# Kernel tuning notes

Hardware: AMD Instinct MI355X
Metric: run time of the kernel (lower is better)

Reference implementation:

```python
import jax, jax.numpy as jnp
import numpy as np

G = 4          # num_groups == num_kv_groups


def _proj(W, b, xf):
    # 1x1 Conv3d == per-voxel linear: xf is [b, c, N]
    return jnp.einsum('oc,bcn->bon', W, xf) + b[None, :, None]


def setup_inputs() -> dict:
    key = jax.random.key(0)
    ks = jax.random.split(key, 5)
    c = 512
    x = jax.random.normal(ks[0], (2, c, 16, 16, 16), dtype=jnp.float32)
    s = 1.0 / np.sqrt(c)
    Wq = jax.random.normal(ks[1], (c, c), dtype=jnp.float32) * s
    Wk = jax.random.normal(ks[2], (c, c), dtype=jnp.float32) * s
    Wv = jax.random.normal(ks[3], (c, c), dtype=jnp.float32) * s
    Wo = jax.random.normal(ks[4], (c, c), dtype=jnp.float32) * s
    z = jnp.zeros((c,), dtype=jnp.float32)
    return {"x": x, "Wq": Wq, "bq": z, "Wk": Wk, "bk": z, "Wv": Wv, "bv": z, "Wo": Wo, "bo": z}


def reference(x, Wq, bq, Wk, bk, Wv, bv, Wo, bo):
    b, c, d, h, w = x.shape
    N = d * h * w
    gs = c // G                       # head (group) dim
    scale = gs ** -0.5
    xf = x.reshape(b, c, N)           # [b, c, N]
    q = _proj(Wq, bq, xf).reshape(b, G, gs, N).transpose(0, 1, 3, 2)  # [b,G,N,gs]
    k = _proj(Wk, bk, xf).reshape(b, G, gs, N).transpose(0, 1, 3, 2)
    v = _proj(Wv, bv, xf).reshape(b, G, gs, N).transpose(0, 1, 3, 2)
    sim = jnp.einsum('bgqd,bgkd->bgqk', q, k) * scale  # [b,G,N,N]
    attn = jax.nn.softmax(sim, axis=-1)
    out = jnp.einsum('bgqk,bgkd->bgqd', attn, v)       # [b,G,N,gs]
    out = out.transpose(0, 1, 3, 2).reshape(b, c, N)   # [b,c,N]
    out = _proj(Wo, bo, out).reshape(b, c, d, h, w)
    return x + out
```

## Files before the change

### kernel.cpp

```cpp
#include <hip/hip_runtime.h>
#include <hip/hip_bf16.h>
#include <stdint.h>

#define B_ 2
#define C_ 512
#define G_ 4
#define D_ 128
#define N_ 4096

typedef __bf16 bf16;
typedef __bf16 bf16x8 __attribute__((ext_vector_type(8)));
typedef float  f32x4  __attribute__((ext_vector_type(4)));
typedef float  f32x16 __attribute__((ext_vector_type(16)));

#define MFMA   __builtin_amdgcn_mfma_f32_16x16x32_bf16
#define MFMA32 __builtin_amdgcn_mfma_f32_32x32x16_bf16

#define SWZ(row, c) ((((c) ^ (((row) >> 1) & 3)) << 4))

#define OFF_Q   (0u)
#define OFF_K   (8388608u)
#define OFF_VT  (16777216u)
#define OFF_XT  (25165824u)
#define OFF_WB  (33554432u)
#define OFF_OP  (35651584u)
#define OFF_ML  (52428800u)
#define WS_NEED_SPLIT (52953088u)

__device__ inline unsigned pk2(float a, float b) {
    union { bf16 h[2]; unsigned u; } t;
    t.h[0] = (bf16)a; t.h[1] = (bf16)b;
    return t.u;
}
__device__ inline void pl32(unsigned &a, unsigned &b) {
    asm volatile("v_permlane32_swap_b32 %0, %1" : "+v"(a), "+v"(b));
}
__device__ inline void gload16(const char* src, char* lds) {
    __builtin_amdgcn_global_load_lds(
        (const __attribute__((address_space(1))) unsigned*)src,
        (__attribute__((address_space(3))) unsigned*)lds, 16, 0, 0);
}
__device__ inline float max3f(float a, float b, float c) {
    return fmaxf(fmaxf(a, b), c);
}

__global__ __launch_bounds__(256) void wcvt_kernel(const float* __restrict__ Wq,
                                                   const float* __restrict__ Wk,
                                                   const float* __restrict__ Wv,
                                                   const float* __restrict__ Wo,
                                                   bf16* __restrict__ out) {
    int m = blockIdx.y;
    const float* W = (m == 0) ? Wq : (m == 1) ? Wk : (m == 2) ? Wv : Wo;
    int i = (blockIdx.x * 256 + threadIdx.x) * 4;
    float4 v = *(const float4*)(W + i);
    union { bf16 h[4]; uint2 u; } pk;
    pk.h[0] = (bf16)v.x; pk.h[1] = (bf16)v.y; pk.h[2] = (bf16)v.z; pk.h[3] = (bf16)v.w;
    *(uint2*)(out + (size_t)m * (C_ * C_) + i) = pk.u;
}

__global__ __launch_bounds__(256) void xt_kernel(const float* __restrict__ x,
                                                 bf16* __restrict__ xT) {
    __shared__ bf16 t[64 * 80];
    int n0 = blockIdx.x * 64, c0 = blockIdx.y * 64, b = blockIdx.z;
    const float* xp = x + (size_t)b * C_ * N_;
#pragma unroll
    for (int i = 0; i < 16; ++i) {
        int idx = threadIdx.x + 256 * i;
        int cl = idx >> 6, nl = idx & 63;
        float v = xp[(size_t)(c0 + cl) * N_ + n0 + nl];
        t[nl * 80 + cl] = (bf16)v;
    }
    __syncthreads();
    bf16* xt = xT + ((size_t)b * N_ + n0) * C_ + c0;
#pragma unroll
    for (int i = 0; i < 2; ++i) {
        int id = threadIdx.x + 256 * i;
        int nl = id >> 3, c8 = (id & 7) * 8;
        *(uint4*)(xt + (size_t)nl * C_ + c8) = *(const uint4*)(t + nl * 80 + c8);
    }
}

__global__ __launch_bounds__(256) void qkv_kernel(const bf16* __restrict__ xT,
                                                  const bf16* __restrict__ WB,
                                                  const float* __restrict__ bq,
                                                  const float* __restrict__ bk,
                                                  const float* __restrict__ bv,
                                                  bf16* __restrict__ Q,
                                                  bf16* __restrict__ K,
                                                  bf16* __restrict__ Vt) {
    __shared__ char smem[32768];
    const int tid = threadIdx.x;
    const int w = tid >> 6, l = tid & 63;
    const int lr = l & 15, lg = l >> 4;
    const int wr = w >> 1, wc = w & 1;
    const int mat = blockIdx.z;
    const bf16* A = xT;
    const bf16* W = WB + (size_t)mat * (C_ * C_);
    const float* bias = (mat == 0) ? bq : (mat == 1) ? bk : bv;
    const int r0 = blockIdx.x * 128, o0 = blockIdx.y * 128;
    const float QSCALE = 0.08838834764831845f * 1.4426950408889634f;

    const char* srcA[2]; const char* srcB[2]; int dA[2], dB[2];
#pragma unroll
    for (int i = 0; i < 2; ++i) {
        int CL = tid + 256 * i, row = CL >> 2, c = CL & 3;
        srcA[i] = (const char*)(A + (size_t)(r0 + row) * C_) + SWZ(row, c);
        srcB[i] = (const char*)(W + (size_t)(o0 + row) * C_) + SWZ(row, c);
        dA[i] = CL << 4;
        dB[i] = 8192 + (CL << 4);
    }

    f32x4 z = {0.f, 0.f, 0.f, 0.f};
    f32x4 acc[4][4];
#pragma unroll
    for (int m = 0; m < 4; ++m)
#pragma unroll
        for (int n = 0; n < 4; ++n) acc[m][n] = z;

    auto STAGE = [&](int buf, int kt) {
        char* base = smem + buf * 16384;
        int kb = kt * 64;
#pragma unroll
        for (int i = 0; i < 2; ++i) {
            gload16(srcA[i] + kb, base + dA[i]);
            gload16(srcB[i] + kb, base + dB[i]);
        }
    };

    STAGE(0, 0);
    __syncthreads();
#pragma unroll 4
    for (int t = 0; t < 16; ++t) {
        int cur = t & 1;
        if (t < 15) STAGE(cur ^ 1, t + 1);
        char* Ab = smem + cur * 16384;
        char* Bb = Ab + 8192;
        bf16x8 af[4], bg_[4];
#pragma unroll
        for (int m = 0; m < 4; ++m) {
            int row = wr * 64 + m * 16 + lr;
            af[m] = *(const bf16x8*)(Ab + row * 64 + SWZ(row, lg));
        }
#pragma unroll
        for (int n = 0; n < 4; ++n) {
            int row = wc * 64 + n * 16 + lr;
            bg_[n] = *(const bf16x8*)(Bb + row * 64 + SWZ(row, lg));
        }
#pragma unroll
        for (int m = 0; m < 4; ++m)
#pragma unroll
            for (int n = 0; n < 4; ++n)
                acc[m][n] = MFMA(af[m], bg_[n], acc[m][n], 0, 0, 0);
        __syncthreads();
    }

#pragma unroll
    for (int n = 0; n < 4; ++n) {
        int o = o0 + wc * 64 + n * 16 + lr;
        float bs = bias[o];
        int g = o >> 7, d = o & 127;
#pragma unroll
        for (int m = 0; m < 4; ++m) {
            int row = r0 + wr * 64 + m * 16 + lg * 4;
            int b = row >> 12, nn = row & (N_ - 1);
            if (mat == 0) {
#pragma unroll
                for (int j = 0; j < 4; ++j)
                    Q[((size_t)(b * G_ + g) * N_ + nn + j) * D_ + d] =
                        (bf16)((acc[m][n][j] + bs) * QSCALE);
            } else if (mat == 1) {
#pragma unroll
                for (int j = 0; j < 4; ++j)
                    K[((size_t)(b * G_ + g) * N_ + nn + j) * D_ + d] =
                        (bf16)(acc[m][n][j] + bs);
            } else {
                union { bf16 h[4]; uint2 u; } pk;
#pragma unroll
                for (int j = 0; j < 4; ++j) pk.h[j] = (bf16)(acc[m][n][j] + bs);
                *(uint2*)(Vt + ((size_t)(b * G_ + g) * D_ + d) * N_ + nn) = pk.u;
            }
        }
    }
}

template<int SPLITS>
__global__ __launch_bounds__(512, 2) void attn_kernel(const bf16* __restrict__ Q,
                                                      const bf16* __restrict__ K,
                                                      const bf16* __restrict__ Vt,
                                                      bf16* __restrict__ XT,
                                                      bf16* __restrict__ Op,
                                                      float* __restrict__ ML) {
    __shared__ char smem[65536];
    const int tid = threadIdx.x;
    const int w = tid >> 6, l = tid & 63;
    const int l31 = l & 31, h = l >> 5;

    const int L = blockIdx.x;
    const int bg = L & 7;
    const int ix = L >> 3;
    const int sp = (SPLITS > 1) ? (ix >> 4) : 0;
    const int qb = (SPLITS > 1) ? (ix & 15) : ix;

    const bf16* Qh = Q + (size_t)bg * N_ * D_;
    const char* Kh = (const char*)(K + (size_t)bg * N_ * D_);
    const char* Vh = (const char*)(Vt + (size_t)bg * D_ * N_);
    const int q0 = qb * 256 + w * 32;
    const int kv0 = sp * (N_ / SPLITS);
    const int NT = N_ / SPLITS / 64;

    int offK[2], offV[2];
#pragma unroll
    for (int j = 0; j < 2; ++j) {
        int CL = (w * 2 + j) * 64 + l;
        int row = CL >> 4;
        int cp = (CL & 15) ^ (row & 15);
        offK[j] = row * 256 + cp * 16;
        int dv = 2 * row + (cp >> 3), k8 = cp & 7;
        offV[j] = dv * (N_ * 2) + k8 * 16;
    }

    bf16x8 aq[8];
#pragma unroll
    for (int kb = 0; kb < 8; ++kb)
        aq[kb] = *(const bf16x8*)(Qh + (size_t)(q0 + l31) * D_ + kb * 16 + h * 8);

    bf16 one_ = (bf16)1.0f;
    bf16x8 ones = {one_, one_, one_, one_, one_, one_, one_, one_};

    f32x16 oacc[4], lacc;
#pragma unroll
    for (int dt = 0; dt < 4; ++dt)
#pragma unroll
        for (int r = 0; r < 16; ++r) oacc[dt][r] = 0.f;
#pragma unroll
    for (int r = 0; r < 16; ++r) lacc[r] = 0.f;
    float mrun = -1e30f;
    const float THR = 5.0f;

    auto STAGE = [&](int buf, int kv) {
        const char* pk = Kh + (size_t)kv * 256;
        const char* pv = Vh + (size_t)kv * 2;
        char* kb = smem + buf * 32768 + w * 2048;
        char* vb = smem + buf * 32768 + 16384 + w * 2048;
#pragma unroll
        for (int j = 0; j < 2; ++j) gload16(pk + offK[j], kb + j * 1024);
#pragma unroll
        for (int j = 0; j < 2; ++j) gload16(pv + offV[j], vb + j * 1024);
    };

    STAGE(0, kv0);

    for (int t = 0; t < NT; ++t) {
        int cur = t & 1;
        __builtin_amdgcn_s_barrier();
        if (t + 1 < NT) {
            STAGE(cur ^ 1, kv0 + (t + 1) * 64);
            asm volatile("s_waitcnt vmcnt(4)" ::: "memory");
        } else {
            asm volatile("s_waitcnt vmcnt(0)" ::: "memory");
        }
        __builtin_amdgcn_sched_barrier(0);
        __builtin_amdgcn_s_barrier();
        char* Kb = smem + cur * 32768;
        char* Vb = smem + cur * 32768 + 16384;

        f32x16 s0, s1;
#pragma unroll
        for (int r = 0; r < 16; ++r) { s0[r] = 0.f; s1[r] = 0.f; }
        __builtin_amdgcn_s_setprio(1);
#pragma unroll
        for (int kb = 0; kb < 8; ++kb) {
            int ch = (((kb << 1) | h) ^ (l31 & 15)) << 4;
            bf16x8 kf0 = *(const bf16x8*)(Kb + (size_t)l31 * 256 + ch);
            s0 = MFMA32(kf0, aq[kb], s0, 0, 0, 0);
            bf16x8 kf1 = *(const bf16x8*)(Kb + (size_t)(32 + l31) * 256 + ch);
            s1 = MFMA32(kf1, aq[kb], s1, 0, 0, 0);
        }
        __builtin_amdgcn_s_setprio(0);

        float x0 = max3f(s0[0],  s0[1],  s0[2]);
        float x1 = max3f(s0[3],  s0[4],  s0[5]);
        float x2 = max3f(s0[6],  s0[7],  s0[8]);
        float x3 = max3f(s0[9],  s0[10], s0[11]);
        float x4 = max3f(s0[12], s0[13], s0[14]);
        float x5 = max3f(s0[15], s1[0],  s1[1]);
        float x6 = max3f(s1[2],  s1[3],  s1[4]);
        float x7 = max3f(s1[5],  s1[6],  s1[7]);
        float x8 = max3f(s1[8],  s1[9],  s1[10]);
        float x9 = max3f(s1[11], s1[12], s1[13]);
        float xa = fmaxf(s1[14], s1[15]);
        float y0 = max3f(x0, x1, x2);
        float y1 = max3f(x3, x4, x5);
        float y2 = max3f(x6, x7, x8);
        float y3 = fmaxf(x9, xa);
        float mt = fmaxf(max3f(y0, y1, y2), y3);
        mt = fmaxf(mt, __shfl_xor(mt, 32));

        if (__any(mt > mrun + THR)) {
            float mn = fmaxf(mrun, mt);
            float corr = __builtin_amdgcn_exp2f(mrun - mn);
            mrun = mn;
#pragma unroll
            for (int r = 0; r < 16; ++r) {
                int qr = (r & 3) + 8 * (r >> 2) + 4 * h;
                float cr = __shfl(corr, qr);
                lacc[r] *= cr;
#pragma unroll
                for (int dt = 0; dt < 4; ++dt) oacc[dt][r] *= cr;
            }
        }

#pragma unroll
        for (int r = 0; r < 16; ++r) {
            s0[r] = __builtin_amdgcn_exp2f(s0[r] - mrun);
            s1[r] = __builtin_amdgcn_exp2f(s1[r] - mrun);
        }

        bf16x8 pa0, pa1, pa2, pa3;
        {
            unsigned x0_ = pk2(s0[0], s0[1]),  y0_ = pk2(s0[4], s0[5]);  pl32(x0_, y0_);
            unsigned x1_ = pk2(s0[2], s0[3]),  y1_ = pk2(s0[6], s0[7]);  pl32(x1_, y1_);
            pa0 = __builtin_bit_cast(bf16x8, (uint4){x0_, x1_, y0_, y1_});
            unsigned x2_ = pk2(s0[8], s0[9]),  y2_ = pk2(s0[12], s0[13]); pl32(x2_, y2_);
            unsigned x3_ = pk2(s0[10], s0[11]), y3_ = pk2(s0[14], s0[15]); pl32(x3_, y3_);
            pa1 = __builtin_bit_cast(bf16x8, (uint4){x2_, x3_, y2_, y3_});
            unsigned x4_ = pk2(s1[0], s1[1]),  y4_ = pk2(s1[4], s1[5]);  pl32(x4_, y4_);
            unsigned x5_ = pk2(s1[2], s1[3]),  y5_ = pk2(s1[6], s1[7]);  pl32(x5_, y5_);
            pa2 = __builtin_bit_cast(bf16x8, (uint4){x4_, x5_, y4_, y5_});
            unsigned x6_ = pk2(s1[8], s1[9]),  y6_ = pk2(s1[12], s1[13]); pl32(x6_, y6_);
            unsigned x7_ = pk2(s1[10], s1[11]), y7_ = pk2(s1[14], s1[15]); pl32(x7_, y7_);
            pa3 = __builtin_bit_cast(bf16x8, (uint4){x6_, x7_, y6_, y7_});
        }

        __builtin_amdgcn_s_setprio(1);
#pragma unroll
        for (int sl = 0; sl < 4; ++sl) {
            bf16x8 pa = (sl == 0) ? pa0 : (sl == 1) ? pa1 : (sl == 2) ? pa2 : pa3;
#pragma unroll
            for (int dt = 0; dt < 4; ++dt) {
                int row = dt * 16 + (l31 >> 1);
                int ch = ((((l31 & 1) << 3) + (sl << 1) + h) ^ (l31 >> 1)) << 4;
                bf16x8 vf = *(const bf16x8*)(Vb + (size_t)row * 256 + ch);
                oacc[dt] = MFMA32(pa, vf, oacc[dt], 0, 0, 0);
            }
            lacc = MFMA32(pa, ones, lacc, 0, 0, 0);
        }
        __builtin_amdgcn_s_setprio(0);
    }

    if (SPLITS > 1) {
        float2* mlp = (float2*)ML + ((size_t)sp * 8 + bg) * N_ + q0;
#pragma unroll
        for (int r = 0; r < 16; ++r) {
            int qr = (r & 3) + 8 * (r >> 2) + 4 * h;
            float mv = __shfl(mrun, qr);
            if (l31 == 0) {
                float2 v; v.x = mv; v.y = lacc[r];
                mlp[qr] = v;
            }
        }
        bf16* op = Op + (((size_t)sp * 8 + bg) * N_ + q0) * D_;
#pragma unroll
        for (int dt = 0; dt < 4; ++dt)
#pragma unroll
            for (int r = 0; r < 16; ++r) {
                int qr = (r & 3) + 8 * (r >> 2) + 4 * h;
                op[(size_t)qr * D_ + dt * 32 + l31] = (bf16)oacc[dt][r];
            }
    } else {
        int b = bg >> 2, g = bg & 3;
#pragma unroll
        for (int r = 0; r < 16; ++r) {
            int qr = (r & 3) + 8 * (r >> 2) + 4 * h;
            float iv = 1.f / lacc[r];
#pragma unroll
            for (int dt = 0; dt < 4; ++dt)
                XT[((size_t)b * N_ + q0 + qr) * C_ + g * D_ + dt * 32 + l31] =
                    (bf16)(oacc[dt][r] * iv);
        }
    }
}

template<int FUSE>
__global__ __launch_bounds__(256) void oproj_kernel(const bf16* __restrict__ Ob,
                                                    const bf16* __restrict__ Op,
                                                    const float* __restrict__ ML,
                                                    const bf16* __restrict__ WB,
                                                    const float* __restrict__ bo,
                                                    const float* __restrict__ x,
                                                    float* __restrict__ out) {
    __shared__ char smem[24576];
    const int tid = threadIdx.x;
    const int w = tid >> 6, l = tid & 63;
    const int lr = l & 15, lg = l >> 4;
    const int wr = w >> 1, wc = w & 1;
    const bf16* W = WB + (size_t)3 * (C_ * C_);
    const int r0 = blockIdx.x * 128, o0 = blockIdx.y * 64;

    const char* srcA[2]; int dA[2], cpw[2]; size_t opRow[2];
    float w0f[2][4], w1f[2][4];
#pragma unroll
    for (int i = 0; i < 2; ++i) {
        int CL = tid + 256 * i, row = CL >> 2, c = CL & 3;
        cpw[i] = c ^ ((row >> 1) & 3);
        dA[i] = CL << 4;
        srcA[i] = (const char*)(Ob + (size_t)(r0 + row) * C_) + (cpw[i] << 4);
        if (FUSE) {
            int rg = r0 + row;
            int b = rg >> 12, n = rg & (N_ - 1);
            const float2* mlp = (const float2*)ML;
#pragma unroll
            for (int g = 0; g < 4; ++g) {
                int bg = b * 4 + g;
                float2 ml0 = mlp[(size_t)bg * N_ + n];
                float2 ml1 = mlp[(size_t)(8 + bg) * N_ + n];
                float mm = fmaxf(ml0.x, ml1.x);
                float a0 = __builtin_amdgcn_exp2f(ml0.x - mm);
                float a1 = __builtin_amdgcn_exp2f(ml1.x - mm);
                float inv = 1.f / (a0 * ml0.y + a1 * ml1.y);
                w0f[i][g] = a0 * inv;
                w1f[i][g] = a1 * inv;
            }
            opRow[i] = ((size_t)(b * 4) * N_ + n) * 256u;
        }
    }
    const char* srcB; int dB;
    {
        int CL = tid, row = CL >> 2, c = CL & 3;
        srcB = (const char*)(W + (size_t)(o0 + row) * C_) + SWZ(row, c);
        dB = 8192 + (CL << 4);
    }

    f32x4 z = {0.f, 0.f, 0.f, 0.f};
    f32x4 acc[4][2];
#pragma unroll
    for (int m = 0; m < 4; ++m) { acc[m][0] = z; acc[m][1] = z; }

    uint4 a0r[2], a1r[2];
    auto LOAD_A = [&](int kt) {
        int g = kt >> 2;
#pragma unroll
        for (int i = 0; i < 2; ++i) {
            size_t off = opRow[i] + (size_t)g * ((size_t)N_ * 256u - 256u)
                       + (size_t)(kt * 64) + ((size_t)cpw[i] << 4);
            a0r[i] = *(const uint4*)((const char*)Op + off);
            a1r[i] = *(const uint4*)((const char*)Op + 8388608u + off);
        }
    };
    auto WRITE_A = [&](int buf, int kt) {
        int g = kt >> 2;
        char* base = smem + buf * 12288;
#pragma unroll
        for (int i = 0; i < 2; ++i) {
            union { uint4 u; bf16 h[8]; } u0, u1, uo;
            u0.u = a0r[i]; u1.u = a1r[i];
#pragma unroll
            for (int e = 0; e < 8; ++e)
                uo.h[e] = (bf16)(w0f[i][g] * (float)u0.h[e] + w1f[i][g] * (float)u1.h[e]);
            *(uint4*)(base + dA[i]) = uo.u;
        }
    };
    auto STAGE_A_PLAIN = [&](int buf, int kt) {
        char* base = smem + buf * 12288;
#pragma unroll
        for (int i = 0; i < 2; ++i) gload16(srcA[i] + kt * 64, base + dA[i]);
    };
    auto STAGE_B = [&](int buf, int kt) {
        gload16(srcB + kt * 64, smem + buf * 12288 + dB);
    };

    STAGE_B(0, 0);
    if (FUSE) { LOAD_A(0); WRITE_A(0, 0); }
    else       STAGE_A_PLAIN(0, 0);
    __syncthreads();

    for (int t = 0; t < 16; ++t) {
        int cur = t & 1;
        if (t < 15) {
            STAGE_B(cur ^ 1, t + 1);
            if (FUSE) LOAD_A(t + 1);
            else      STAGE_A_PLAIN(cur ^ 1, t + 1);
        }
        char* Ab = smem + cur * 12288;
        char* Bb = Ab + 8192;
        bf16x8 af[4], bg_[2];
#pragma unroll
        for (int m = 0; m < 4; ++m) {
            int row = wr * 64 + m * 16 + lr;
            af[m] = *(const bf16x8*)(Ab + row * 64 + SWZ(row, lg));
        }
#pragma unroll
        for (int n = 0; n < 2; ++n) {
            int row = wc * 32 + n * 16 + lr;
            bg_[n] = *(const bf16x8*)(Bb + row * 64 + SWZ(row, lg));
        }
#pragma unroll
        for (int m = 0; m < 4; ++m)
#pragma unroll
            for (int n = 0; n < 2; ++n)
                acc[m][n] = MFMA(af[m], bg_[n], acc[m][n], 0, 0, 0);
        if (FUSE && t < 15) WRITE_A(cur ^ 1, t + 1);
        __syncthreads();
    }

#pragma unroll
    for (int n = 0; n < 2; ++n) {
        int o = o0 + wc * 32 + n * 16 + lr;
        float bs = bo[o];
#pragma unroll
        for (int m = 0; m < 4; ++m) {
            int row = r0 + wr * 64 + m * 16 + lg * 4;
            int b = row >> 12, nn = row & (N_ - 1);
            size_t base = ((size_t)b * C_ + o) * N_ + nn;
            float4 xv = *(const float4*)(x + base);
            float4 ov;
            ov.x = acc[m][n][0] + bs + xv.x;
            ov.y = acc[m][n][1] + bs + xv.y;
            ov.z = acc[m][n][2] + bs + xv.z;
            ov.w = acc[m][n][3] + bs + xv.w;
            *(float4*)(out + base) = ov;
        }
    }
}

extern "C" void kernel_launch(void* const* d_in, const int* in_sizes, int n_in,
                              void* d_out, int out_size, void* d_ws, size_t ws_size,
                              hipStream_t stream) {
    const float* x  = (const float*)d_in[0];
    const float* Wq = (const float*)d_in[1];
    const float* bq = (const float*)d_in[2];
    const float* Wk = (const float*)d_in[3];
    const float* bk = (const float*)d_in[4];
    const float* Wv = (const float*)d_in[5];
    const float* bv = (const float*)d_in[6];
    const float* Wo = (const float*)d_in[7];
    const float* bo = (const float*)d_in[8];

    char* ws = (char*)d_ws;
    bf16* Q   = (bf16*)(ws + OFF_Q);
    bf16* K   = (bf16*)(ws + OFF_K);
    bf16* Vt  = (bf16*)(ws + OFF_VT);
    bf16* XT  = (bf16*)(ws + OFF_XT);
    bf16* WB  = (bf16*)(ws + OFF_WB);
    bf16* Op  = (bf16*)(ws + OFF_OP);
    float* ML = (float*)(ws + OFF_ML);
    float* out = (float*)d_out;

    hipLaunchKernelGGL(wcvt_kernel, dim3(256, 4), dim3(256), 0, stream, Wq, Wk, Wv, Wo, WB);
    hipLaunchKernelGGL(xt_kernel, dim3(64, 8, 2), dim3(256), 0, stream, x, XT);
    hipLaunchKernelGGL(qkv_kernel, dim3(64, 4, 3), dim3(256), 0, stream,
                       XT, WB, bq, bk, bv, Q, K, Vt);
    if (ws_size >= (size_t)WS_NEED_SPLIT) {
        hipLaunchKernelGGL(attn_kernel<2>, dim3(256), dim3(512), 0, stream,
                           Q, K, Vt, XT, Op, ML);
        hipLaunchKernelGGL(oproj_kernel<1>, dim3(64, 8), dim3(256), 0, stream,
                           XT, Op, ML, WB, bo, x, out);
    } else {
        hipLaunchKernelGGL(attn_kernel<1>, dim3(128), dim3(512), 0, stream,
                           Q, K, Vt, XT, Op, ML);
        hipLaunchKernelGGL(oproj_kernel<0>, dim3(64, 8), dim3(256), 0, stream,
                           XT, Op, ML, WB, bo, x, out);
    }
}
```

Baseline: 131.9 us.

## Stage 128-key KV tiles per barrier in new big-LDS attention kernel

Adds an attention kernel that uses 128KB of dynamic shared memory to double-buffer 128-key KV chunks, so each pair of barriers covers two 64-key sub-tiles. The goal is to halve the barrier and wait count per key and keep more loads in flight. In exchange occupancy drops to one 512-thread block per CU instead of two, which may reduce latency hiding across blocks. The tile body is factored into shared helpers, and the old kernel remains as a fallback if the shared-memory attribute cannot be set.

```diff
diff --git a/kernel.cpp b/kernel.cpp
--- a/kernel.cpp
+++ b/kernel.cpp
@@ -183,6 +183,123 @@
     }
 }
 
+struct AttnState {
+    f32x16 oacc[4], lacc;
+    float mrun;
+};
+
+template<typename T>
+__device__ inline void attn_tile_body(AttnState& st, const bf16x8* aq,
+                                      const bf16x8& ones, char* Kb, char* Vb,
+                                      int l31, int h, T) {
+    const float THR = 5.0f;
+    f32x16 s0, s1;
+#pragma unroll
+    for (int r = 0; r < 16; ++r) { s0[r] = 0.f; s1[r] = 0.f; }
+    __builtin_amdgcn_s_setprio(1);
+#pragma unroll
+    for (int kb = 0; kb < 8; ++kb) {
+        int ch = (((kb << 1) | h) ^ (l31 & 15)) << 4;
+        bf16x8 kf0 = *(const bf16x8*)(Kb + (size_t)l31 * 256 + ch);
+        s0 = MFMA32(kf0, aq[kb], s0, 0, 0, 0);
+        bf16x8 kf1 = *(const bf16x8*)(Kb + (size_t)(32 + l31) * 256 + ch);
+        s1 = MFMA32(kf1, aq[kb], s1, 0, 0, 0);
+    }
+    __builtin_amdgcn_s_setprio(0);
+
+    float x0 = max3f(s0[0],  s0[1],  s0[2]);
+    float x1 = max3f(s0[3],  s0[4],  s0[5]);
+    float x2 = max3f(s0[6],  s0[7],  s0[8]);
+    float x3 = max3f(s0[9],  s0[10], s0[11]);
+    float x4 = max3f(s0[12], s0[13], s0[14]);
+    float x5 = max3f(s0[15], s1[0],  s1[1]);
+    float x6 = max3f(s1[2],  s1[3],  s1[4]);
+    float x7 = max3f(s1[5],  s1[6],  s1[7]);
+    float x8 = max3f(s1[8],  s1[9],  s1[10]);
+    float x9 = max3f(s1[11], s1[12], s1[13]);
+    float xa = fmaxf(s1[14], s1[15]);
+    float y0 = max3f(x0, x1, x2);
+    float y1 = max3f(x3, x4, x5);
+    float y2 = max3f(x6, x7, x8);
+    float y3 = fmaxf(x9, xa);
+    float mt = fmaxf(max3f(y0, y1, y2), y3);
+    mt = fmaxf(mt, __shfl_xor(mt, 32));
+
+    if (__any(mt > st.mrun + THR)) {
+        float mn = fmaxf(st.mrun, mt);
+        float corr = __builtin_amdgcn_exp2f(st.mrun - mn);
+        st.mrun = mn;
+#pragma unroll
+        for (int r = 0; r < 16; ++r) {
+            int qr = (r & 3) + 8 * (r >> 2) + 4 * h;
+            float cr = __shfl(corr, qr);
+            st.lacc[r] *= cr;
+#pragma unroll
+            for (int dt = 0; dt < 4; ++dt) st.oacc[dt][r] *= cr;
+        }
+    }
+
+#pragma unroll
+    for (int r = 0; r < 16; ++r) {
+        s0[r] = __builtin_amdgcn_exp2f(s0[r] - st.mrun);
+        s1[r] = __builtin_amdgcn_exp2f(s1[r] - st.mrun);
+    }
+
+    bf16x8 pa0, pa1, pa2, pa3;
+    {
+        unsigned u0 = pk2(s0[0], s0[1]),  v0 = pk2(s0[4], s0[5]);  pl32(u0, v0);
+        unsigned u1 = pk2(s0[2], s0[3]),  v1 = pk2(s0[6], s0[7]);  pl32(u1, v1);
+        pa0 = __builtin_bit_cast(bf16x8, (uint4){u0, u1, v0, v1});
+        unsigned u2 = pk2(s0[8], s0[9]),  v2 = pk2(s0[12], s0[13]); pl32(u2, v2);
+        unsigned u3 = pk2(s0[10], s0[11]), v3 = pk2(s0[14], s0[15]); pl32(u3, v3);
+        pa1 = __builtin_bit_cast(bf16x8, (uint4){u2, u3, v2, v3});
+        unsigned u4 = pk2(s1[0], s1[1]),  v4 = pk2(s1[4], s1[5]);  pl32(u4, v4);
+        unsigned u5 = pk2(s1[2], s1[3]),  v5 = pk2(s1[6], s1[7]);  pl32(u5, v5);
+        pa2 = __builtin_bit_cast(bf16x8, (uint4){u4, u5, v4, v5});
+        unsigned u6 = pk2(s1[8], s1[9]),  v6 = pk2(s1[12], s1[13]); pl32(u6, v6);
+        unsigned u7 = pk2(s1[10], s1[11]), v7 = pk2(s1[14], s1[15]); pl32(u7, v7);
+        pa3 = __builtin_bit_cast(bf16x8, (uint4){u6, u7, v6, v7});
+    }
+
+    __builtin_amdgcn_s_setprio(1);
+#pragma unroll
+    for (int sl = 0; sl < 4; ++sl) {
+        bf16x8 pa = (sl == 0) ? pa0 : (sl == 1) ? pa1 : (sl == 2) ? pa2 : pa3;
+#pragma unroll
+        for (int dt = 0; dt < 4; ++dt) {
+            int row = dt * 16 + (l31 >> 1);
+            int ch = ((((l31 & 1) << 3) + (sl << 1) + h) ^ (l31 >> 1)) << 4;
+            bf16x8 vf = *(const bf16x8*)(Vb + (size_t)row * 256 + ch);
+            st.oacc[dt] = MFMA32(pa, vf, st.oacc[dt], 0, 0, 0);
+        }
+        st.lacc = MFMA32(pa, ones, st.lacc, 0, 0, 0);
+    }
+    __builtin_amdgcn_s_setprio(0);
+}
+
+__device__ inline void attn_epilogue(AttnState& st, int sp, int bg, int q0,
+                                     int l, int l31, int h,
+                                     bf16* Op, float* ML) {
+    float2* mlp = (float2*)ML + ((size_t)sp * 8 + bg) * N_ + q0;
+#pragma unroll
+    for (int r = 0; r < 16; ++r) {
+        int qr = (r & 3) + 8 * (r >> 2) + 4 * h;
+        float mv = __shfl(st.mrun, qr);
+        if (l31 == 0) {
+            float2 v; v.x = mv; v.y = st.lacc[r];
+            mlp[qr] = v;
+        }
+    }
+    bf16* op = Op + (((size_t)sp * 8 + bg) * N_ + q0) * D_;
+#pragma unroll
+    for (int dt = 0; dt < 4; ++dt)
+#pragma unroll
+        for (int r = 0; r < 16; ++r) {
+            int qr = (r & 3) + 8 * (r >> 2) + 4 * h;
+            op[(size_t)qr * D_ + dt * 32 + l31] = (bf16)st.oacc[dt][r];
+        }
+}
+
 template<int SPLITS>
 __global__ __launch_bounds__(512, 2) void attn_kernel(const bf16* __restrict__ Q,
                                                       const bf16* __restrict__ K,
@@ -227,15 +344,14 @@
     bf16 one_ = (bf16)1.0f;
     bf16x8 ones = {one_, one_, one_, one_, one_, one_, one_, one_};
 
-    f32x16 oacc[4], lacc;
+    AttnState st;
 #pragma unroll
     for (int dt = 0; dt < 4; ++dt)
 #pragma unroll
-        for (int r = 0; r < 16; ++r) oacc[dt][r] = 0.f;
-#pragma unroll
-    for (int r = 0; r < 16; ++r) lacc[r] = 0.f;
-    float mrun = -1e30f;
-    const float THR = 5.0f;
+        for (int r = 0; r < 16; ++r) st.oacc[dt][r] = 0.f;
+#pragma unroll
+    for (int r = 0; r < 16; ++r) st.lacc[r] = 0.f;
+    st.mrun = -1e30f;
 
     auto STAGE = [&](int buf, int kv) {
         const char* pk = Kh + (size_t)kv * 256;
@@ -261,124 +377,112 @@
         }
         __builtin_amdgcn_sched_barrier(0);
         __builtin_amdgcn_s_barrier();
-        char* Kb = smem + cur * 32768;
-        char* Vb = smem + cur * 32768 + 16384;
-
-        f32x16 s0, s1;
-#pragma unroll
-        for (int r = 0; r < 16; ++r) { s0[r] = 0.f; s1[r] = 0.f; }
-        __builtin_amdgcn_s_setprio(1);
-#pragma unroll
-        for (int kb = 0; kb < 8; ++kb) {
-            int ch = (((kb << 1) | h) ^ (l31 & 15)) << 4;
-            bf16x8 kf0 = *(const bf16x8*)(Kb + (size_t)l31 * 256 + ch);
-            s0 = MFMA32(kf0, aq[kb], s0, 0, 0, 0);
-            bf16x8 kf1 = *(const bf16x8*)(Kb + (size_t)(32 + l31) * 256 + ch);
-            s1 = MFMA32(kf1, aq[kb], s1, 0, 0, 0);
-        }
-        __builtin_amdgcn_s_setprio(0);
-
-        float x0 = max3f(s0[0],  s0[1],  s0[2]);
-        float x1 = max3f(s0[3],  s0[4],  s0[5]);
-        float x2 = max3f(s0[6],  s0[7],  s0[8]);
-        float x3 = max3f(s0[9],  s0[10], s0[11]);
-        float x4 = max3f(s0[12], s0[13], s0[14]);
-        float x5 = max3f(s0[15], s1[0],  s1[1]);
-        float x6 = max3f(s1[2],  s1[3],  s1[4]);
-        float x7 = max3f(s1[5],  s1[6],  s1[7]);
-        float x8 = max3f(s1[8],  s1[9],  s1[10]);
-        float x9 = max3f(s1[11], s1[12], s1[13]);
-        float xa = fmaxf(s1[14], s1[15]);
-        float y0 = max3f(x0, x1, x2);
-        float y1 = max3f(x3, x4, x5);
-        float y2 = max3f(x6, x7, x8);
-        float y3 = fmaxf(x9, xa);
-        float mt = fmaxf(max3f(y0, y1, y2), y3);
-        mt = fmaxf(mt, __shfl_xor(mt, 32));
-
-        if (__any(mt > mrun + THR)) {
-            float mn = fmaxf(mrun, mt);
-            float corr = __builtin_amdgcn_exp2f(mrun - mn);
-            mrun = mn;
-#pragma unroll
-            for (int r = 0; r < 16; ++r) {
-                int qr = (r & 3) + 8 * (r >> 2) + 4 * h;
-                float cr = __shfl(corr, qr);
-                lacc[r] *= cr;
-#pragma unroll
-                for (int dt = 0; dt < 4; ++dt) oacc[dt][r] *= cr;
-            }
-        }
-
-#pragma unroll
-        for (int r = 0; r < 16; ++r) {
-            s0[r] = __builtin_amdgcn_exp2f(s0[r] - mrun);
-            s1[r] = __builtin_amdgcn_exp2f(s1[r] - mrun);
-        }
-
-        bf16x8 pa0, pa1, pa2, pa3;
-        {
-            unsigned x0_ = pk2(s0[0], s0[1]),  y0_ = pk2(s0[4], s0[5]);  pl32(x0_, y0_);
-            unsigned x1_ = pk2(s0[2], s0[3]),  y1_ = pk2(s0[6], s0[7]);  pl32(x1_, y1_);
-            pa0 = __builtin_bit_cast(bf16x8, (uint4){x0_, x1_, y0_, y1_});
-            unsigned x2_ = pk2(s0[8], s0[9]),  y2_ = pk2(s0[12], s0[13]); pl32(x2_, y2_);
-            unsigned x3_ = pk2(s0[10], s0[11]), y3_ = pk2(s0[14], s0[15]); pl32(x3_, y3_);
-            pa1 = __builtin_bit_cast(bf16x8, (uint4){x2_, x3_, y2_, y3_});
-            unsigned x4_ = pk2(s1[0], s1[1]),  y4_ = pk2(s1[4], s1[5]);  pl32(x4_, y4_);
-            unsigned x5_ = pk2(s1[2], s1[3]),  y5_ = pk2(s1[6], s1[7]);  pl32(x5_, y5_);
-            pa2 = __builtin_bit_cast(bf16x8, (uint4){x4_, x5_, y4_, y5_});
-            unsigned x6_ = pk2(s1[8], s1[9]),  y6_ = pk2(s1[12], s1[13]); pl32(x6_, y6_);
-            unsigned x7_ = pk2(s1[10], s1[11]), y7_ = pk2(s1[14], s1[15]); pl32(x7_, y7_);
-            pa3 = __builtin_bit_cast(bf16x8, (uint4){x6_, x7_, y6_, y7_});
-        }
-
-        __builtin_amdgcn_s_setprio(1);
-#pragma unroll
-        for (int sl = 0; sl < 4; ++sl) {
-            bf16x8 pa = (sl == 0) ? pa0 : (sl == 1) ? pa1 : (sl == 2) ? pa2 : pa3;
-#pragma unroll
-            for (int dt = 0; dt < 4; ++dt) {
-                int row = dt * 16 + (l31 >> 1);
-                int ch = ((((l31 & 1) << 3) + (sl << 1) + h) ^ (l31 >> 1)) << 4;
-                bf16x8 vf = *(const bf16x8*)(Vb + (size_t)row * 256 + ch);
-                oacc[dt] = MFMA32(pa, vf, oacc[dt], 0, 0, 0);
-            }
-            lacc = MFMA32(pa, ones, lacc, 0, 0, 0);
-        }
-        __builtin_amdgcn_s_setprio(0);
+        attn_tile_body(st, aq, ones, smem + cur * 32768,
+                       smem + cur * 32768 + 16384, l31, h, 0);
     }
 
     if (SPLITS > 1) {
-        float2* mlp = (float2*)ML + ((size_t)sp * 8 + bg) * N_ + q0;
+        attn_epilogue(st, sp, bg, q0, l, l31, h, Op, ML);
+    } else {
+        int b = bg >> 2, g = bg & 3;
 #pragma unroll
         for (int r = 0; r < 16; ++r) {
             int qr = (r & 3) + 8 * (r >> 2) + 4 * h;
-            float mv = __shfl(mrun, qr);
-            if (l31 == 0) {
-                float2 v; v.x = mv; v.y = lacc[r];
-                mlp[qr] = v;
-            }
-        }
-        bf16* op = Op + (((size_t)sp * 8 + bg) * N_ + q0) * D_;
-#pragma unroll
-        for (int dt = 0; dt < 4; ++dt)
-#pragma unroll
-            for (int r = 0; r < 16; ++r) {
-                int qr = (r & 3) + 8 * (r >> 2) + 4 * h;
-                op[(size_t)qr * D_ + dt * 32 + l31] = (bf16)oacc[dt][r];
-            }
-    } else {
-        int b = bg >> 2, g = bg & 3;
-#pragma unroll
-        for (int r = 0; r < 16; ++r) {
-            int qr = (r & 3) + 8 * (r >> 2) + 4 * h;
-            float iv = 1.f / lacc[r];
+            float iv = 1.f / st.lacc[r];
 #pragma unroll
             for (int dt = 0; dt < 4; ++dt)
                 XT[((size_t)b * N_ + q0 + qr) * C_ + g * D_ + dt * 32 + l31] =
-                    (bf16)(oacc[dt][r] * iv);
-        }
-    }
+                    (bf16)(st.oacc[dt][r] * iv);
+        }
+    }
+}
+
+__global__ __launch_bounds__(512, 1) void attn_big_kernel(const bf16* __restrict__ Q,
+                                                          const bf16* __restrict__ K,
+                                                          const bf16* __restrict__ Vt,
+                                                          bf16* __restrict__ Op,
+                                                          float* __restrict__ ML) {
+    extern __shared__ char smem[];
+    const int tid = threadIdx.x;
+    const int w = tid >> 6, l = tid & 63;
+    const int l31 = l & 31, h = l >> 5;
+
+    const int L = blockIdx.x;
+    const int bg = L & 7;
+    const int ix = L >> 3;
+    const int sp = ix >> 4;
+    const int qb = ix & 15;
+
+    const bf16* Qh = Q + (size_t)bg * N_ * D_;
+    const char* Kh = (const char*)(K + (size_t)bg * N_ * D_);
+    const char* Vh = (const char*)(Vt + (size_t)bg * D_ * N_);
+    const int q0 = qb * 256 + w * 32;
+    const int kv0 = sp * (N_ / 2);
+    const int NT = (N_ / 2) / 128;
+
+    int offK[2], offV[2];
+#pragma unroll
+    for (int j = 0; j < 2; ++j) {
+        int CL = (w * 2 + j) * 64 + l;
+        int row = CL >> 4;
+        int cp = (CL & 15) ^ (row & 15);
+        offK[j] = row * 256 + cp * 16;
+        int dv = 2 * row + (cp >> 3), k8 = cp & 7;
+        offV[j] = dv * (N_ * 2) + k8 * 16;
+    }
+
+    bf16x8 aq[8];
+#pragma unroll
+    for (int kb = 0; kb < 8; ++kb)
+        aq[kb] = *(const bf16x8*)(Qh + (size_t)(q0 + l31) * D_ + kb * 16 + h * 8);
+
+    bf16 one_ = (bf16)1.0f;
+    bf16x8 ones = {one_, one_, one_, one_, one_, one_, one_, one_};
+
+    AttnState st;
+#pragma unroll
+    for (int dt = 0; dt < 4; ++dt)
+#pragma unroll
+        for (int r = 0; r < 16; ++r) st.oacc[dt][r] = 0.f;
+#pragma unroll
+    for (int r = 0; r < 16; ++r) st.lacc[r] = 0.f;
+    st.mrun = -1e30f;
+
+    auto STAGE = [&](int buf, int kv) {
+#pragma unroll
+        for (int s2 = 0; s2 < 2; ++s2) {
+            const char* pk = Kh + (size_t)(kv + 64 * s2) * 256;
+            const char* pv = Vh + (size_t)(kv + 64 * s2) * 2;
+            char* kb = smem + buf * 65536 + s2 * 16384 + w * 2048;
+            char* vb = smem + buf * 65536 + 32768 + s2 * 16384 + w * 2048;
+#pragma unroll
+            for (int j = 0; j < 2; ++j) gload16(pk + offK[j], kb + j * 1024);
+#pragma unroll
+            for (int j = 0; j < 2; ++j) gload16(pv + offV[j], vb + j * 1024);
+        }
+    };
+
+    STAGE(0, kv0);
+
+    for (int t = 0; t < NT; ++t) {
+        int cur = t & 1;
+        __builtin_amdgcn_s_barrier();
+        if (t + 1 < NT) {
+            STAGE(cur ^ 1, kv0 + (t + 1) * 128);
+            asm volatile("s_waitcnt vmcnt(8)" ::: "memory");
+        } else {
+            asm volatile("s_waitcnt vmcnt(0)" ::: "memory");
+        }
+        __builtin_amdgcn_sched_barrier(0);
+        __builtin_amdgcn_s_barrier();
+#pragma unroll
+        for (int s2 = 0; s2 < 2; ++s2)
+            attn_tile_body(st, aq, ones,
+                           smem + cur * 65536 + s2 * 16384,
+                           smem + cur * 65536 + 32768 + s2 * 16384, l31, h, 0);
+    }
+
+    attn_epilogue(st, sp, bg, q0, l, l31, h, Op, ML);
 }
 
 template<int FUSE>
@@ -551,8 +655,16 @@
     hipLaunchKernelGGL(qkv_kernel, dim3(64, 4, 3), dim3(256), 0, stream,
                        XT, WB, bq, bk, bv, Q, K, Vt);
     if (ws_size >= (size_t)WS_NEED_SPLIT) {
-        hipLaunchKernelGGL(attn_kernel<2>, dim3(256), dim3(512), 0, stream,
-                           Q, K, Vt, XT, Op, ML);
+        hipError_t e = hipFuncSetAttribute(
+            reinterpret_cast<const void*>(&attn_big_kernel),
+            hipFuncAttributeMaxDynamicSharedMemorySize, 131072);
+        if (e == hipSuccess) {
+            hipLaunchKernelGGL(attn_big_kernel, dim3(256), dim3(512), 131072, stream,
+                               Q, K, Vt, Op, ML);
+        } else {
+            hipLaunchKernelGGL(attn_kernel<2>, dim3(256), dim3(512), 0, stream,
+                               Q, K, Vt, XT, Op, ML);
+        }
         hipLaunchKernelGGL(oproj_kernel<1>, dim3(64, 8), dim3(256), 0, stream,
                            XT, Op, ML, WB, bo, x, out);
     } else {
```

Measured after the change: 130.5 us. Within noise of the previous version (-1.1%).
